# Performance work log

Measured on AMD Instinct MI355X. Metric: run time of the kernel, lower is better.

## Reference

```python
import jax, jax.numpy as jnp
import numpy as np

IGNORE_INDEX = -100
N, C = 2097152, 32


def setup_inputs() -> dict:
    key = jax.random.key(0)
    k1, k2, k3 = jax.random.split(key, 3)
    pred = jax.random.normal(k1, (N, C), dtype=jnp.float32)
    # neg_count (~0.95N) > pos_num * factor (~0.15N).
    r = jax.random.randint(k2, (N,), 0, 100, dtype=jnp.int32)
    cls = jax.random.randint(k3, (N,), 1, C, dtype=jnp.int32)
    label = jnp.where(r >= 95, cls, 0).astype(jnp.int32)
    return {"pred": pred, "label": label, "factor": 3}


def reference(pred, label, factor):
    n = pred.shape[0]
    is_pos = label != 0
    pos_num = jnp.sum(is_pos)
    neg_sum = pos_num * factor
    num_neg = n - pos_num

    # max non-background score per row
    pred_value = jnp.max(pred[:, 1:], axis=1)  # [N]

    # descending sort of negative-position scores (positives pushed to the end)
    neg_scores = jnp.where(is_pos, -jnp.inf, pred_value)
    sorted_desc = -jnp.sort(-neg_scores)
    idx = jnp.clip(neg_sum - 1, 0, n - 1)
    threshold = sorted_desc[idx]

    mask_thr = (pred_value >= threshold) | is_pos
    mask_all = label != -1
    mask = jnp.where(num_neg > neg_sum, mask_thr, mask_all)
    mask = jax.lax.stop_gradient(mask)  # torch computes mask on detached numpy

    masked_label = jnp.where(mask, label, IGNORE_INDEX)
    valid = masked_label != IGNORE_INDEX
    safe_label = jnp.where(valid, masked_label, 0)

    logp = jax.nn.log_softmax(pred, axis=-1)  # [N, C]
    nll = -jnp.take_along_axis(logp, safe_label[:, None], axis=1)[:, 0]  # [N]
    denom = jnp.maximum(jnp.sum(valid), 1)
    loss = jnp.sum(jnp.where(valid, nll, 0.0)) / denom.astype(pred.dtype)
    return loss
```

## Files before the change

### kernel.cpp

```cpp
#include <hip/hip_runtime.h>


typedef float f4 __attribute__((ext_vector_type(4)));

#define TILE_ROWS 256
#define ROW_F4    9

struct Ctrl {
    unsigned hist8[256];
    unsigned hist12[4096];
    unsigned bcnt[4096];
    float    bsum[4096];
    unsigned pos_num;
    unsigned cnt;
    unsigned done;
    unsigned pad;
    double   sum;
};

__global__ void init_kernel(unsigned* w, int words) {
    for (int i = threadIdx.x + blockIdx.x * blockDim.x; i < words;
         i += blockDim.x * gridDim.x)
        w[i] = 0u;
}

__device__ inline void wave_hist_add(unsigned* h, unsigned bucket) {
    unsigned long long todo = __ballot(1);
    while (todo) {
        int leader = (int)__builtin_ctzll(todo);
        unsigned b = __shfl(bucket, leader);
        unsigned long long same = __ballot(bucket == b) & todo;
        if ((int)(threadIdx.x & 63) == leader)
            atomicAdd(&h[b], (unsigned)__popcll(same));
        todo &= ~same;
    }
}

__global__ void __launch_bounds__(256)
row_kernel(const f4* __restrict__ pred4, const int* __restrict__ label,
           unsigned* __restrict__ keys, float* __restrict__ nll,
           Ctrl* __restrict__ c, int n) {
    __shared__ f4 tile[TILE_ROWS * ROW_F4];
    __shared__ unsigned h[256];
    for (int i = threadIdx.x; i < 256; i += 256) h[i] = 0u;
    __syncthreads();

    const int tid = threadIdx.x;
    int pos_local = 0;
    const int tile_stride = gridDim.x * TILE_ROWS;

    for (int tbase = blockIdx.x * TILE_ROWS; tbase < n; tbase += tile_stride) {
#pragma unroll
        for (int k = 0; k < 8; ++k) {
            int idx = (k << 8) + tid;
            f4 v = pred4[(size_t)tbase * 8 + idx];
            tile[(idx >> 3) * ROW_F4 + (idx & 7)] = v;
        }
        __syncthreads();

        int row = tbase + tid;
        float r[32];
#pragma unroll
        for (int j = 0; j < 8; ++j) {
            f4 v = tile[tid * ROW_F4 + j];
            r[4 * j + 0] = v.x; r[4 * j + 1] = v.y;
            r[4 * j + 2] = v.z; r[4 * j + 3] = v.w;
        }
        float m_nb = r[1];
#pragma unroll
        for (int j = 2; j < 32; ++j) m_nb = fmaxf(m_nb, r[j]);
        float m_all = fmaxf(m_nb, r[0]);

        float s = 0.f;
#pragma unroll
        for (int j = 0; j < 32; ++j) s += __expf(r[j] - m_all);

        int lab = label[row];
        int sl = lab; sl = sl < 0 ? 0 : sl; sl = sl > 31 ? 31 : sl;
        float xl = r[0];
#pragma unroll
        for (int j = 1; j < 32; ++j) xl = (j == sl) ? r[j] : xl;

        nll[row] = (m_all + __logf(s)) - xl;

        bool is_pos = (lab != 0);
        pos_local += is_pos ? 1 : 0;

        float ns = is_pos ? -__builtin_inff() : m_nb;
        unsigned u    = __float_as_uint(ns);
        unsigned ukey = (u & 0x80000000u) ? ~u : (u | 0x80000000u);
        unsigned dkey = ~ukey;
        keys[row] = dkey;
        wave_hist_add(h, dkey >> 24);

        __syncthreads();
    }

#pragma unroll
    for (int off = 32; off > 0; off >>= 1) pos_local += __shfl_down(pos_local, off);
    __shared__ int wsum[4];
    int wid = threadIdx.x >> 6;
    if ((threadIdx.x & 63) == 0) wsum[wid] = pos_local;
    __syncthreads();
    if (threadIdx.x == 0)
        atomicAdd(&c->pos_num, (unsigned)(wsum[0] + wsum[1] + wsum[2] + wsum[3]));

    for (int i = threadIdx.x; i < 256; i += 256)
        if (h[i]) atomicAdd(&c->hist8[i], h[i]);
}

__device__ inline void block_scan256(unsigned* s) {
    const int t = threadIdx.x;
#pragma unroll
    for (int off = 1; off < 256; off <<= 1) {
        unsigned v = (t >= off) ? s[t - off] : 0u;
        __syncthreads();
        s[t] += v;
        __syncthreads();
    }
}

__device__ inline void rank_params(const Ctrl* c, int factor, int n,
                                   unsigned& rank, bool& use_thr) {
    long long pos     = (long long)c->pos_num;
    long long neg_sum = pos * (long long)factor;
    long long num_neg = (long long)n - pos;
    long long idx     = neg_sum - 1;
    if (idx < 0) idx = 0;
    if (idx > (long long)n - 1) idx = (long long)n - 1;
    rank    = (unsigned)idx;
    use_thr = (num_neg > neg_sum);
}

__device__ inline void select_byte3(const Ctrl* c, unsigned rank, unsigned* s,
                                    unsigned* shbr, unsigned& b3, unsigned& rank1) {
    const int t = threadIdx.x;
    unsigned cnt8 = c->hist8[t];
    s[t] = cnt8;
    __syncthreads();
    block_scan256(s);
    unsigned incl = s[t], excl = incl - cnt8;
    if (cnt8 > 0u && excl <= rank && rank < incl) {
        shbr[0] = (unsigned)t;
        shbr[1] = rank - excl;
    }
    __syncthreads();
    b3 = shbr[0];
    rank1 = shbr[1];
    __syncthreads();
}

__device__ inline void select_12(const unsigned* hist, unsigned rank_in,
                                 unsigned* s, unsigned* shbr,
                                 unsigned& sub, unsigned& rank_out) {
    const int t = threadIdx.x;
    unsigned lc[16]; unsigned lsum = 0u;
#pragma unroll
    for (int i = 0; i < 16; ++i) { lc[i] = hist[t * 16 + i]; lsum += lc[i]; }
    s[t] = lsum;
    __syncthreads();
    block_scan256(s);
    unsigned incl = s[t], excl = incl - lsum;
    if (lsum > 0u && excl <= rank_in && rank_in < incl) {
        unsigned r = rank_in - excl;
#pragma unroll
        for (int i = 0; i < 16; ++i) {
            if (r < lc[i]) { shbr[0] = (unsigned)(t * 16 + i); shbr[1] = r; break; }
            r -= lc[i];
        }
    }
    __syncthreads();
    sub = shbr[0];
    rank_out = shbr[1];
    __syncthreads();
}

__global__ void __launch_bounds__(256)
hist12_kernel(const unsigned* __restrict__ keys, Ctrl* __restrict__ c,
              const int* __restrict__ factor_p, int n) {
    __shared__ unsigned s[256];
    __shared__ unsigned shbr[2];
    __shared__ unsigned h[4096];
    const int t = threadIdx.x;

    unsigned rank; bool use_thr;
    rank_params(c, factor_p[0], n, rank, use_thr);
    unsigned b3, rank1;
    select_byte3(c, rank, s, shbr, b3, rank1);

    for (int i = t; i < 4096; i += 256) h[i] = 0u;
    __syncthreads();

    const int stride = gridDim.x * blockDim.x;
    for (int i = blockIdx.x * blockDim.x + t; i < n; i += stride) {
        unsigned k = keys[i];
        if ((k >> 24) == b3) atomicAdd(&h[(k >> 12) & 0xFFFu], 1u);
    }
    __syncthreads();
    for (int i = t; i < 4096; i += 256)
        if (h[i]) atomicAdd(&c->hist12[i], h[i]);
}

__global__ void __launch_bounds__(256)
reduceF_kernel(const unsigned* __restrict__ keys, const int* __restrict__ label,
               const float* __restrict__ nll, Ctrl* __restrict__ c,
               const int* __restrict__ factor_p, int n, float* __restrict__ out) {
    __shared__ unsigned s[256];
    __shared__ unsigned shbr[2];
    __shared__ double sd[4];
    __shared__ int    si[4];
    const int t = threadIdx.x, lane = t & 63, wid = t >> 6;

    unsigned rank; bool use_thr;
    rank_params(c, factor_p[0], n, rank, use_thr);
    unsigned b3, rank1;
    select_byte3(c, rank, s, shbr, b3, rank1);
    unsigned sub, rank2;
    select_12(c->hist12, rank1, s, shbr, sub, rank2);
    const unsigned prefix20 = (b3 << 12) | sub;

    double local = 0.0;
    int cntl = 0;
    const int stride = gridDim.x * blockDim.x;
    for (int i = blockIdx.x * blockDim.x + t; i < n; i += stride) {
        int lab = label[i];
        float nl = nll[i];
        if (use_thr) {
            unsigned k = keys[i];
            unsigned top20 = k >> 12;
            if (lab != 0 || top20 < prefix20) { local += (double)nl; cntl++; }
            else if (top20 == prefix20) {
                atomicAdd(&c->bcnt[k & 0xFFFu], 1u);
                atomicAdd(&c->bsum[k & 0xFFFu], nl);
            }
        } else {
            if (lab != -1) { local += (double)nl; cntl++; }
        }
    }
#pragma unroll
    for (int off = 32; off > 0; off >>= 1) {
        local += __shfl_down(local, off);
        cntl  += __shfl_down(cntl, off);
    }
    if (lane == 0) { sd[wid] = local; si[wid] = cntl; }
    __syncthreads();
    __shared__ int s_last;
    if (t == 0) {
        atomicAdd(&c->sum, sd[0] + sd[1] + sd[2] + sd[3]);
        atomicAdd(&c->cnt, (unsigned)(si[0] + si[1] + si[2] + si[3]));
        __threadfence();
        unsigned d = atomicAdd(&c->done, 1u);
        s_last = (d == gridDim.x - 1) ? 1 : 0;
    }
    __syncthreads();
    if (!s_last) return;

    __threadfence();
    __shared__ double   fssum;
    __shared__ unsigned fscnt;
    if (t == 0) { fssum = 0.0; fscnt = 0u; }
    __syncthreads();
    if (use_thr) {
        unsigned bstar, dummy;
        select_12(c->bcnt, rank2, s, shbr, bstar, dummy);
        double fsl = 0.0; unsigned fcl = 0u;
        for (int i = t; i < 4096; i += 256)
            if ((unsigned)i <= bstar) { fcl += c->bcnt[i]; fsl += (double)c->bsum[i]; }
#pragma unroll
        for (int off = 32; off > 0; off >>= 1) {
            fsl += __shfl_down(fsl, off);
            fcl += __shfl_down(fcl, off);
        }
        if (lane == 0) { sd[wid] = fsl; si[wid] = (int)fcl; }
        __syncthreads();
        if (t == 0) {
            fssum = sd[0] + sd[1] + sd[2] + sd[3];
            fscnt = (unsigned)(si[0] + si[1] + si[2] + si[3]);
        }
        __syncthreads();
    }
    if (t == 0) {
        double sm = c->sum + fssum;
        unsigned ctn = c->cnt + fscnt;
        double denom = (ctn == 0u) ? 1.0 : (double)ctn;
        out[0] = (float)(sm / denom);
    }
}

extern "C" void kernel_launch(void* const* d_in, const int* in_sizes, int n_in,
                              void* d_out, int out_size, void* d_ws, size_t ws_size,
                              hipStream_t stream) {
    const float* pred = (const float*)d_in[0];
    const int* label  = (const int*)d_in[1];
    const int* factor = (const int*)d_in[2];
    int n = in_sizes[1];
    float* out = (float*)d_out;

    char* ws = (char*)d_ws;
    Ctrl* c = (Ctrl*)ws;
    unsigned* keys = (unsigned*)(ws + 65536);
    float* nll = (float*)(ws + 65536 + (size_t)n * 4);

    init_kernel<<<64, 256, 0, stream>>>((unsigned*)c, (int)(sizeof(Ctrl) / 4));
    row_kernel<<<2048, 256, 0, stream>>>((const f4*)pred, label, keys, nll, c, n);
    hist12_kernel<<<1024, 256, 0, stream>>>(keys, c, factor, n);
    reduceF_kernel<<<1024, 256, 0, stream>>>(keys, label, nll, c, factor, n, out);
}
```

Measured before the change: 144.6 us.

## Shrink row tiles, swizzle block order, split reductions, skip label reads in reduce

```diff
diff --git a/kernel.cpp b/kernel.cpp
--- a/kernel.cpp
+++ b/kernel.cpp
@@ -3,8 +3,10 @@
 
 typedef float f4 __attribute__((ext_vector_type(4)));
 
-#define TILE_ROWS 256
-#define ROW_F4    9
+#define TILE_ROWS   128
+#define ROW_F4      9
+#define ROW_THREADS 128
+#define ROW_BLOCKS  4096
 
 struct Ctrl {
     unsigned hist8[256];
@@ -36,23 +38,27 @@
     }
 }
 
-__global__ void __launch_bounds__(256)
+__global__ void __launch_bounds__(ROW_THREADS)
 row_kernel(const f4* __restrict__ pred4, const int* __restrict__ label,
            unsigned* __restrict__ keys, float* __restrict__ nll,
            Ctrl* __restrict__ c, int n) {
     __shared__ f4 tile[TILE_ROWS * ROW_F4];
     __shared__ unsigned h[256];
-    for (int i = threadIdx.x; i < 256; i += 256) h[i] = 0u;
-    __syncthreads();
-
+    __shared__ int wsum[2];
     const int tid = threadIdx.x;
+    h[tid] = 0u; h[tid + 128] = 0u;
+    __syncthreads();
+
+    const unsigned B   = gridDim.x;
+    const unsigned swz = (blockIdx.x & 7u) * (B >> 3) + (blockIdx.x >> 3);
+
+    const int tile_stride = B * TILE_ROWS;
     int pos_local = 0;
-    const int tile_stride = gridDim.x * TILE_ROWS;
-
-    for (int tbase = blockIdx.x * TILE_ROWS; tbase < n; tbase += tile_stride) {
+
+    for (int tbase = (int)swz * TILE_ROWS; tbase < n; tbase += tile_stride) {
 #pragma unroll
         for (int k = 0; k < 8; ++k) {
-            int idx = (k << 8) + tid;
+            int idx = (k << 7) + tid;
             f4 v = pred4[(size_t)tbase * 8 + idx];
             tile[(idx >> 3) * ROW_F4 + (idx & 7)] = v;
         }
@@ -66,22 +72,29 @@
             r[4 * j + 0] = v.x; r[4 * j + 1] = v.y;
             r[4 * j + 2] = v.z; r[4 * j + 3] = v.w;
         }
-        float m_nb = r[1];
-#pragma unroll
-        for (int j = 2; j < 32; ++j) m_nb = fmaxf(m_nb, r[j]);
+        float m0 = r[1], m1 = r[2], m2 = r[3], m3 = r[4];
+#pragma unroll
+        for (int j = 5; j <= 28; j += 4) {
+            m0 = fmaxf(m0, r[j]);   m1 = fmaxf(m1, r[j+1]);
+            m2 = fmaxf(m2, r[j+2]); m3 = fmaxf(m3, r[j+3]);
+        }
+        m0 = fmaxf(m0, r[29]); m1 = fmaxf(m1, r[30]); m2 = fmaxf(m2, r[31]);
+        float m_nb  = fmaxf(fmaxf(m0, m1), fmaxf(m2, m3));
         float m_all = fmaxf(m_nb, r[0]);
 
-        float s = 0.f;
-#pragma unroll
-        for (int j = 0; j < 32; ++j) s += __expf(r[j] - m_all);
+        float s0 = 0.f, s1 = 0.f, s2 = 0.f, s3 = 0.f;
+#pragma unroll
+        for (int j = 0; j < 32; j += 4) {
+            s0 += __expf(r[j]   - m_all);  s1 += __expf(r[j+1] - m_all);
+            s2 += __expf(r[j+2] - m_all);  s3 += __expf(r[j+3] - m_all);
+        }
+        float ssum = (s0 + s1) + (s2 + s3);
 
         int lab = label[row];
         int sl = lab; sl = sl < 0 ? 0 : sl; sl = sl > 31 ? 31 : sl;
-        float xl = r[0];
-#pragma unroll
-        for (int j = 1; j < 32; ++j) xl = (j == sl) ? r[j] : xl;
-
-        nll[row] = (m_all + __logf(s)) - xl;
+        float xl = ((const float*)tile)[tid * (ROW_F4 * 4) + sl];
+
+        nll[row] = (m_all + __logf(ssum)) - xl;
 
         bool is_pos = (lab != 0);
         pos_local += is_pos ? 1 : 0;
@@ -97,16 +110,14 @@
     }
 
 #pragma unroll
-    for (int off = 32; off > 0; off >>= 1) pos_local += __shfl_down(pos_local, off);
-    __shared__ int wsum[4];
-    int wid = threadIdx.x >> 6;
-    if ((threadIdx.x & 63) == 0) wsum[wid] = pos_local;
-    __syncthreads();
-    if (threadIdx.x == 0)
-        atomicAdd(&c->pos_num, (unsigned)(wsum[0] + wsum[1] + wsum[2] + wsum[3]));
-
-    for (int i = threadIdx.x; i < 256; i += 256)
-        if (h[i]) atomicAdd(&c->hist8[i], h[i]);
+    for (int off = 32; off > 0; off >>= 1)
+        pos_local += __shfl_down(pos_local, off);
+    if ((tid & 63) == 0) wsum[tid >> 6] = pos_local;
+    __syncthreads();
+    if (tid == 0)
+        atomicAdd(&c->pos_num, (unsigned)(wsum[0] + wsum[1]));
+    if (h[tid])       atomicAdd(&c->hist8[tid],       h[tid]);
+    if (h[tid + 128]) atomicAdd(&c->hist8[tid + 128], h[tid + 128]);
 }
 
 __device__ inline void block_scan256(unsigned* s) {
@@ -215,26 +226,27 @@
     rank_params(c, factor_p[0], n, rank, use_thr);
     unsigned b3, rank1;
     select_byte3(c, rank, s, shbr, b3, rank1);
-    unsigned sub, rank2;
-    select_12(c->hist12, rank1, s, shbr, sub, rank2);
+    unsigned sub = 0u, rank2 = 0u;
+    if (use_thr) select_12(c->hist12, rank1, s, shbr, sub, rank2);
     const unsigned prefix20 = (b3 << 12) | sub;
 
     double local = 0.0;
     int cntl = 0;
     const int stride = gridDim.x * blockDim.x;
-    for (int i = blockIdx.x * blockDim.x + t; i < n; i += stride) {
-        int lab = label[i];
-        float nl = nll[i];
-        if (use_thr) {
+    if (use_thr) {
+        for (int i = blockIdx.x * blockDim.x + t; i < n; i += stride) {
             unsigned k = keys[i];
+            float nl = nll[i];
             unsigned top20 = k >> 12;
-            if (lab != 0 || top20 < prefix20) { local += (double)nl; cntl++; }
+            if (k == 0xFF800000u || top20 < prefix20) { local += (double)nl; cntl++; }
             else if (top20 == prefix20) {
                 atomicAdd(&c->bcnt[k & 0xFFFu], 1u);
                 atomicAdd(&c->bsum[k & 0xFFFu], nl);
             }
-        } else {
-            if (lab != -1) { local += (double)nl; cntl++; }
+        }
+    } else {
+        for (int i = blockIdx.x * blockDim.x + t; i < n; i += stride) {
+            if (label[i] != -1) { local += (double)nll[i]; cntl++; }
         }
     }
 #pragma unroll
@@ -302,7 +314,8 @@
     float* nll = (float*)(ws + 65536 + (size_t)n * 4);
 
     init_kernel<<<64, 256, 0, stream>>>((unsigned*)c, (int)(sizeof(Ctrl) / 4));
-    row_kernel<<<2048, 256, 0, stream>>>((const f4*)pred, label, keys, nll, c, n);
+    row_kernel<<<ROW_BLOCKS, ROW_THREADS, 0, stream>>>((const f4*)pred, label,
+                                                       keys, nll, c, n);
     hist12_kernel<<<1024, 256, 0, stream>>>(keys, c, factor, n);
     reduceF_kernel<<<1024, 256, 0, stream>>>(keys, label, nll, c, factor, n, out);
 }
```

Result: slower. 165.5 us (+14.4%).
